# Optimization experiments

Hardware: AMD Instinct MI355X
Metric: run time of the kernel (lower is better)

## Reference

```python
import jax, jax.numpy as jnp
import numpy as np

D_MODEL = 1024
D_STATE = 16
D_CONV = 4
EXPAND = 2
D_INNER = D_MODEL * EXPAND


def soft_clamp(x, lo, hi, sharp):
    c = (hi + lo) / 2.0
    r = (hi - lo) / 2.0
    return jnp.tanh((x - c) / (r + 1e-8) * sharp) / sharp * r + c


def setup_inputs() -> dict:
    key = jax.random.key(0)
    ks = jax.random.split(key, 9)
    B, L = 2, 1024
    x = jax.random.normal(ks[0], (B, L, D_MODEL), jnp.float32)
    norm_w = jnp.ones((D_MODEL,), jnp.float32)
    W_in = jax.random.normal(ks[1], (2 * D_INNER, D_MODEL), jnp.float32) * 0.02
    conv_w = jax.random.normal(ks[2], (D_INNER, 1, D_CONV), jnp.float32) * 0.02
    conv_b = jnp.zeros((D_INNER,), jnp.float32)
    W_dt = jax.random.normal(ks[3], (D_INNER, D_INNER), jnp.float32) * 0.02
    b_dt = jnp.full((D_INNER,), -2.0, jnp.float32)
    W_B = jax.random.normal(ks[4], (D_STATE, D_INNER), jnp.float32) * 0.02
    W_C = jax.random.normal(ks[5], (D_STATE, D_INNER), jnp.float32) * 0.02
    A_log = jax.random.normal(ks[6], (D_INNER, D_STATE), jnp.float32) * 0.1
    D_param = jnp.full((D_INNER,), 0.1, jnp.float32)
    W_out = jax.random.normal(ks[7], (D_MODEL, D_INNER), jnp.float32) * 0.02
    residual_scale = jnp.asarray(0.3, jnp.float32)
    return dict(x=x, norm_w=norm_w, W_in=W_in, conv_w=conv_w, conv_b=conv_b,
                W_dt=W_dt, b_dt=b_dt, W_B=W_B, W_C=W_C, A_log=A_log,
                D_param=D_param, W_out=W_out, residual_scale=residual_scale)


def reference(x, norm_w, W_in, conv_w, conv_b, W_dt, b_dt, W_B, W_C, A_log,
              D_param, W_out, residual_scale):
    B, L, _ = x.shape
    # RMSNorm
    var = jnp.mean(x * x, axis=-1, keepdims=True)
    xn = x * jax.lax.rsqrt(var + 1e-6) * norm_w
    # in_proj, chunk into ssm branch and gate branch
    proj = xn @ W_in.T                              # (B, L, 2*D_INNER)
    x_branch, gate = proj[..., :D_INNER], proj[..., D_INNER:]
    # depthwise causal conv1d (padding=d_conv-1 then slice == left pad)
    xc = jax.lax.conv_general_dilated(
        jnp.swapaxes(x_branch, 1, 2), conv_w, (1,), [(D_CONV - 1, 0)],
        dimension_numbers=('NCH', 'OIH', 'NCH'), feature_group_count=D_INNER)
    xc = xc + conv_b[None, :, None]
    xc = jnp.swapaxes(xc, 1, 2)                     # (B, L, D_INNER)
    xc = xc * jax.nn.sigmoid(xc)                    # SiLU
    # selective SSM parameterization
    dt = soft_clamp(jax.nn.softplus(xc @ W_dt.T + b_dt), 1e-3, 0.1, 0.5)
    Bp = xc @ W_B.T                                 # (B, L, N)
    Cp = xc @ W_C.T                                 # (B, L, N)
    A = -jnp.exp(soft_clamp(A_log, -5.0, 5.0, 0.5))  # (D, N)
    dt_A = soft_clamp(dt[..., None] * A[None, None], -8.0, 8.0, 0.5)
    dA = jnp.exp(dt_A)                              # (B, L, D, N)
    dB = dt[..., None] * Bp[:, :, None, :]          # (B, L, D, N)

    h0 = jnp.zeros((B, D_INNER, D_STATE), jnp.float32)

    def step(h, inp):
        dA_t, dB_t, x_t, C_t, t = inp
        h = h * dA_t + dB_t * x_t[:, :, None]
        # every 10 steps: rescale if ||h|| > 20 (factor==1 otherwise)
        nrm = jnp.sqrt(jnp.sum(h * h, axis=(1, 2), keepdims=True))
        fac = jnp.minimum(20.0 / (nrm + 1e-8), 1.0)
        h = jnp.where(t % 10 == 0, h * fac, h)
        y = jnp.einsum('bdn,bn->bd', h, C_t) + D_param * x_t
        return h, y

    xs = (jnp.swapaxes(dA, 0, 1), jnp.swapaxes(dB, 0, 1),
          jnp.swapaxes(xc, 0, 1), jnp.swapaxes(Cp, 0, 1), jnp.arange(L))
    _, ys = jax.lax.scan(step, h0, xs)
    x_ssm = jnp.swapaxes(ys, 0, 1)                  # (B, L, D_INNER)

    x_out = (x_ssm * (gate * jax.nn.sigmoid(gate))) @ W_out.T
    scale = jax.nn.sigmoid(residual_scale) * 0.5
    return x + scale * x_out
```

## Files before the change

### kernel.cpp

```cpp
#include <hip/hip_runtime.h>
#include <hip/hip_bf16.h>
#include <math.h>

#define B_   2
#define L_   1024
#define DM   1024
#define DI   2048
#define DS   16
#define M_   (B_*L_)
#define TCH  64
#define NCH  16
#define NCHAIN (B_*DI*DS)

typedef __hip_bfloat16 bf16;
typedef __attribute__((ext_vector_type(8))) short short8;
typedef __attribute__((ext_vector_type(4))) float f32x4;

__device__ __forceinline__ float bf2f(bf16 v){ return __bfloat162float(v); }
__device__ __forceinline__ bf16  f2bf(float v){ return __float2bfloat16(v); }
__device__ __forceinline__ float s2f(short v){ bf16 b; *(short*)&b = v; return bf2f(b); }
__device__ __forceinline__ short f2s(float v){ bf16 b = f2bf(v); return *(short*)&b; }

__device__ __forceinline__ float ftanh(float x){
  float e = __expf(-2.f*fabsf(x));
  float t = (1.f-e)/(1.f+e);
  return x < 0.f ? -t : t;
}
__device__ __forceinline__ float fsoftplus(float x){
  return fmaxf(x,0.f) + log1pf(__expf(-fabsf(x)));
}
__device__ __forceinline__ float soft_clamp(float x, float lo, float hi){
  float c = 0.5f*(hi+lo), r = 0.5f*(hi-lo);
  float u = (x-c)/(r+1e-8f)*0.5f;
  return ftanh(u)*2.f*r + c;
}

#define NT 13
struct SrcPtrs { const void* p[NT]; };

static constexpr size_t CUM[NT+1] = {
  0,
  2097152,
  2098176,
  6292480,
  6300672,
  6302720,
  10497024,
  10499072,
  10531840,
  10564608,
  10597376,
  10599424,
  12696576,
  12696577
};
#define TOTELEM 12696577
#define CVTBLK  ((TOTELEM - 2097152 + 255)/256)

__global__ __launch_bounds__(256) void prep_k(SrcPtrs sp, bf16* __restrict__ arena,
                                              bf16* __restrict__ xn){
  __shared__ float wsum[4];
  const bool isbf = (((const unsigned short*)sp.p[1])[0] == 0x3F80u);
  if (blockIdx.x < M_){
    const int row = blockIdx.x;
    const int t   = threadIdx.x;
    float f[4];
    if (isbf){
      const bf16* xr = (const bf16*)sp.p[0] + (size_t)row*DM;
      #pragma unroll
      for (int i=0;i<4;i++) f[i] = bf2f(xr[t*4+i]);
    } else {
      const float* xr = (const float*)sp.p[0] + (size_t)row*DM;
      f32x4 v = *(const f32x4*)&xr[t*4];
      #pragma unroll
      for (int i=0;i<4;i++) f[i] = v[i];
    }
    float ss = f[0]*f[0]+f[1]*f[1]+f[2]*f[2]+f[3]*f[3];
    #pragma unroll
    for (int s=32;s;s>>=1) ss += __shfl_xor(ss, s, 64);
    if ((t & 63) == 0) wsum[t>>6] = ss;
    __syncthreads();
    float tot = wsum[0]+wsum[1]+wsum[2]+wsum[3];
    float rr  = rsqrtf(tot*(1.f/DM) + 1e-6f);
    float wv[4];
    if (isbf){
      const bf16* wp = (const bf16*)sp.p[1];
      #pragma unroll
      for (int i=0;i<4;i++) wv[i] = bf2f(wp[t*4+i]);
    } else {
      f32x4 v = *(const f32x4*)((const float*)sp.p[1] + t*4);
      #pragma unroll
      for (int i=0;i<4;i++) wv[i] = v[i];
    }
    bf16* o = xn + (size_t)row*DM;
    #pragma unroll
    for (int i=0;i<4;i++) o[t*4+i] = f2bf(f[i]*rr*wv[i]);
  } else {
    size_t i = (size_t)(blockIdx.x - M_)*256 + threadIdx.x + CUM[1];
    if (i >= TOTELEM) return;
    int s = 1;
    #pragma unroll
    for (int k=2;k<NT;k++) if (i >= CUM[k]) s = k;
    size_t loc = i - CUM[s];
    float v = isbf ? bf2f(((const bf16*)sp.p[s])[loc])
                   : ((const float*)sp.p[s])[loc];
    arena[i] = f2bf(v);
  }
}

__device__ __forceinline__ void gload16(const bf16* g, short* l){
  __builtin_amdgcn_global_load_lds((const __attribute__((address_space(1))) void*)g,
                                   (__attribute__((address_space(3))) void*)l, 16, 0, 0);
}

template<int EPI, int BM, int BN, int WR, int WC>
__global__ __launch_bounds__(256)
void gemm_bt(const bf16* __restrict__ A, const bf16* __restrict__ Bw,
             bf16* __restrict__ Cb,
             const int M, const int Ncols, const int K,
             const bf16* __restrict__ bias,
             const void* __restrict__ xraw,
             const bf16* __restrict__ rsp,
             void* __restrict__ outraw,
             const unsigned short* __restrict__ probe,
             float* __restrict__ BpOut, float* __restrict__ CpOut){
  constexpr int WM   = BM/WR, WN = BN/WC;
  constexpr int MI   = WM/16, NJ = WN/16;
  constexpr int ROWS = BM + BN;
  constexpr int STG  = ROWS*32/2048;
  __shared__ __align__(16) short ls[2][ROWS*32];
  const int tid  = threadIdx.x;
  const int lane = tid & 63;
  const int w    = tid >> 6;
  const int wr   = (w / WC) * WM;
  const int wc   = (w % WC) * WN;
  const int lc   = lane & 15;
  const int kb   = (lane >> 4) * 8;
  int bx, by;
  if (EPI == 1){
    const int flat = blockIdx.x;
    if (flat < 512){ bx = flat & 31; by = flat >> 5; }
    else           { bx = 32;        by = flat - 512; }
  } else { bx = blockIdx.x; by = blockIdx.y; }
  const int m0   = by * BM;
  const int n0   = bx * BN;

  auto stage = [&](int kk, int b){
    #pragma unroll
    for (int r=0;r<STG;r++){
      const int idx = r*2048 + tid*8;
      const int row = idx >> 5, col = idx & 31;
      const bf16* src = (row < BM) ? (A  + (size_t)(m0 + row)*K + kk + col)
                                   : (Bw + (size_t)(n0 + row - BM)*K + kk + col);
      gload16(src, &ls[b][idx]);
    }
  };

  f32x4 acc[MI][NJ] = {};

  stage(0, 0);
  int cur = 0;
  for (int k0 = 0; k0 < K; k0 += 32){
    __syncthreads();
    if (k0 + 32 < K) stage(k0 + 32, cur^1);
    short8 af[MI], bfv[NJ];
    #pragma unroll
    for (int i=0;i<MI;i++) af[i]  = *(const short8*)&ls[cur][(wr + i*16 + lc)*32 + kb];
    #pragma unroll
    for (int j=0;j<NJ;j++) bfv[j] = *(const short8*)&ls[cur][(BM + wc + j*16 + lc)*32 + kb];
    #pragma unroll
    for (int i=0;i<MI;i++)
      #pragma unroll
      for (int j=0;j<NJ;j++)
        acc[i][j] = __builtin_amdgcn_mfma_f32_16x16x32_bf16(af[i], bfv[j], acc[i][j], 0, 0, 0);
    cur ^= 1;
  }

  const int lr = lane >> 4;
  float scale = 0.f;
  bool isbf = true;
  if (EPI == 2){
    scale = 0.5f / (1.f + __expf(-bf2f(rsp[0])));
    isbf  = (probe[0] == 0x3F80u);
  }
  #pragma unroll
  for (int i=0;i<MI;i++){
    #pragma unroll
    for (int j=0;j<NJ;j++){
      const int gm0 = m0 + wr + i*16 + lr*4;
      const int gn  = n0 + wc + j*16 + lc;
      #pragma unroll
      for (int r=0;r<4;r++){
        float v = acc[i][j][r];
        const int gm = gm0 + r;
        if (EPI == 0){
          Cb[(size_t)gm*Ncols + gn] = f2bf(v);
        } else if (EPI == 1){
          if (gn < 2048){
            float z = fsoftplus(v + bf2f(bias[gn]));
            Cb[(size_t)gm*2048 + gn] = f2bf(soft_clamp(z, 0.001f, 0.1f));
          } else if (gn >= 2049 && gn < 2065){
            BpOut[gm*16 + (gn-2049)] = v;
          } else if (gn >= 2065 && gn < 2081){
            CpOut[gm*16 + (gn-2065)] = v;
          }
        } else {
          size_t off = (size_t)gm*Ncols + gn;
          if (isbf){
            float xv = bf2f(((const bf16*)xraw)[off]);
            ((bf16*)outraw)[off] = f2bf(xv + scale*v);
          } else {
            float xv = ((const float*)xraw)[off];
            ((float*)outraw)[off] = xv + scale*v;
          }
        }
      }
    }
  }
}

__global__ __launch_bounds__(256) void conv_silu_k(const bf16* __restrict__ proj,
                                                   const bf16* __restrict__ cw,
                                                   const bf16* __restrict__ cb,
                                                   bf16* __restrict__ xc){
  const int idx8 = blockIdx.x*256 + threadIdx.x;
  const int dp   = idx8 & (DI/8 - 1);
  const int row  = idx8 >> 8;
  const int l    = row & (L_-1);
  const int d0   = dp*8;
  short8 vb = *(const short8*)&cb[d0];
  short8 w0 = *(const short8*)&cw[d0*4];
  short8 w1 = *(const short8*)&cw[d0*4+8];
  short8 w2 = *(const short8*)&cw[d0*4+16];
  short8 w3 = *(const short8*)&cw[d0*4+24];
  float s[8];
  #pragma unroll
  for (int i=0;i<8;i++) s[i] = s2f(vb[i]);
  #pragma unroll
  for (int k=0;k<4;k++){
    int ll = l - 3 + k;
    if (ll >= 0){
      short8 vp = *(const short8*)&proj[(size_t)(row-3+k)*(2*DI) + d0];
      #pragma unroll
      for (int i=0;i<8;i++){
        const int widx = i*4+k;
        short wv = (widx<8)?w0[widx]:(widx<16)?w1[widx-8]:(widx<24)?w2[widx-16]:w3[widx-24];
        s[i] += s2f(vp[i])*s2f(wv);
      }
    }
  }
  short8 o;
  #pragma unroll
  for (int i=0;i<8;i++) o[i] = f2s(s[i] / (1.f + __expf(-s[i])));
  *(short8*)&xc[(size_t)idx8*8] = o;
}


__global__ __launch_bounds__(64) void scanA_k(const bf16* __restrict__ dtab,
    const bf16* __restrict__ xcb, const float* __restrict__ Bp,
    const bf16* __restrict__ Alog,
    float* __restrict__ Pg, float* __restrict__ Qg){
  __shared__ __align__(16) bf16  sdt[TCH][72];
  __shared__ __align__(16) bf16  sxc[TCH][72];
  __shared__ __align__(16) float sB [TCH][16];
  const int bx   = blockIdx.x;
  const int c    = bx & 15;
  const int dti  = (bx >> 4) & 31;
  const int b    = bx >> 9;
  const int lane = threadIdx.x;
  const int d0   = dti*64, d = d0 + lane;
  const int t0   = c*TCH;
  const size_t bL = (size_t)b*L_;
  #pragma unroll
  for (int i=0;i<8;i++){
    int task = i*64 + lane;
    int t = task >> 3, sub = task & 7;
    size_t g = (bL + t0 + t)*DI + d0 + sub*8;
    *(short8*)&sdt[t][sub*8] = *(const short8*)&dtab[g];
    *(short8*)&sxc[t][sub*8] = *(const short8*)&xcb[g];
  }
  #pragma unroll
  for (int i=0;i<4;i++){
    int task = i*64 + lane;
    int t = task >> 2, sub = task & 3;
    *(f32x4*)&sB[t][sub*4] = *(const f32x4*)&Bp[(bL + t0 + t)*DS + sub*4];
  }
  float Av[16];
  #pragma unroll
  for (int n=0;n<16;n++)
    Av[n] = -__expf(soft_clamp(bf2f(Alog[(size_t)d*DS + n]), -5.f, 5.f));
  __syncthreads();

  float P[16], Q[16];
  #pragma unroll
  for (int n=0;n<16;n++){ P[n]=1.f; Q[n]=0.f; }
  for (int t=0;t<TCH;t++){
    float dtv = bf2f(sdt[t][lane]);
    float xv  = bf2f(sxc[t][lane]);
    float dtx = dtv*xv;
    #pragma unroll
    for (int n=0;n<16;n++){
      float a = __expf(dtv*Av[n]);
      P[n] *= a;
      Q[n] = a*Q[n] + dtx*sB[t][n];
    }
  }
  const size_t base = ((size_t)c*(B_*DI) + (size_t)b*DI + d)*DS;
  #pragma unroll
  for (int n=0;n<16;n+=4){
    f32x4 pv = {P[n],P[n+1],P[n+2],P[n+3]};
    f32x4 qv = {Q[n],Q[n+1],Q[n+2],Q[n+3]};
    *(f32x4*)&Pg[base+n] = pv;
    *(f32x4*)&Qg[base+n] = qv;
  }
}

__global__ __launch_bounds__(64) void scanBC_k(const bf16* __restrict__ dtab,
    const bf16* __restrict__ xcb, const float* __restrict__ Bp,
    const float* __restrict__ Cp, const bf16* __restrict__ Alog,
    const bf16* __restrict__ Dp,
    const float* __restrict__ Pg, const float* __restrict__ Qg,
    const bf16* __restrict__ proj, bf16* __restrict__ aout){
  __shared__ __align__(16) bf16  sdt[TCH][72];
  __shared__ __align__(16) bf16  sxc[TCH][72];
  __shared__ __align__(16) bf16  sg [TCH][72];
  __shared__ __align__(16) float sB [TCH][16];
  __shared__ __align__(16) float sC [TCH][16];
  const int bx   = blockIdx.x;
  const int c    = bx & 15;
  const int dti  = (bx >> 4) & 31;
  const int b    = bx >> 9;
  const int lane = threadIdx.x;
  const int d0   = dti*64, d = d0 + lane;
  const int t0   = c*TCH;
  const size_t bL = (size_t)b*L_;
  #pragma unroll
  for (int i=0;i<8;i++){
    int task = i*64 + lane;
    int t = task >> 3, sub = task & 7;
    size_t g = (bL + t0 + t)*DI + d0 + sub*8;
    *(short8*)&sdt[t][sub*8] = *(const short8*)&dtab[g];
    *(short8*)&sxc[t][sub*8] = *(const short8*)&xcb[g];
    *(short8*)&sg [t][sub*8] = *(const short8*)&proj[(bL + t0 + t)*(2*DI) + DI + d0 + sub*8];
  }
  #pragma unroll
  for (int i=0;i<4;i++){
    int task = i*64 + lane;
    int t = task >> 2, sub = task & 3;
    *(f32x4*)&sB[t][sub*4] = *(const f32x4*)&Bp[(bL + t0 + t)*DS + sub*4];
    *(f32x4*)&sC[t][sub*4] = *(const f32x4*)&Cp[(bL + t0 + t)*DS + sub*4];
  }
  float Av[16];
  #pragma unroll
  for (int n=0;n<16;n++)
    Av[n] = -__expf(soft_clamp(bf2f(Alog[(size_t)d*DS + n]), -5.f, 5.f));
  float h[16];
  #pragma unroll
  for (int n=0;n<16;n++) h[n] = 0.f;
  const size_t chainb = ((size_t)b*DI + d)*DS;
  for (int cc=0; cc<c; cc++){
    const size_t pb = (size_t)cc*(B_*DI*DS) + chainb;
    #pragma unroll
    for (int n=0;n<16;n+=4){
      f32x4 pv = *(const f32x4*)&Pg[pb+n];
      f32x4 qv = *(const f32x4*)&Qg[pb+n];
      #pragma unroll
      for (int k=0;k<4;k++) h[n+k] = pv[k]*h[n+k] + qv[k];
    }
  }
  const float Dv = bf2f(Dp[d]);
  __syncthreads();

  for (int t=0;t<TCH;t++){
    float dtv = bf2f(sdt[t][lane]);
    float xv  = bf2f(sxc[t][lane]);
    float dtx = dtv*xv;
    float y   = Dv*xv;
    #pragma unroll
    for (int n=0;n<16;n++){
      float a = __expf(dtv*Av[n]);
      h[n] = a*h[n] + dtx*sB[t][n];
      y   += h[n]*sC[t][n];
    }
    float gv  = bf2f(sg[t][lane]);
    float sig = 1.f/(1.f + __expf(-gv));
    aout[(bL + t0 + t)*DI + d] = f2bf(y * gv * sig);
  }
}

extern "C" void kernel_launch(void* const* d_in, const int* in_sizes, int n_in,
                              void* d_out, int out_size, void* d_ws, size_t ws_size,
                              hipStream_t stream) {
  SrcPtrs sp;
  for (int i=0;i<NT;i++) sp.p[i] = d_in[i];

  char* ws = (char*)d_ws;
  bf16* arena = (bf16*)ws;  ws += ((size_t)TOTELEM*2 + 255) & ~(size_t)255;
  bf16*  proj = (bf16*)ws;  ws += (size_t)M_*2*DI*2;
  bf16*  xc   = (bf16*)ws;  ws += (size_t)M_*DI*2;
  bf16*  dt   = (bf16*)ws;  ws += (size_t)M_*DI*2;
  float* Bp   = (float*)ws; ws += (size_t)M_*DS*4;
  float* Cp   = (float*)ws; ws += (size_t)M_*DS*4;
  float* Pg   = (float*)ws; ws += (size_t)NCH*NCHAIN*4;
  float* Qg   = (float*)ws; ws += (size_t)NCH*NCHAIN*4;
  bf16*  xn   = (bf16*)Qg;
  bf16*  aout = dt;

  bf16* Win_b  = arena + CUM[2];
  bf16* cw_b   = arena + CUM[3];
  bf16* cb_b   = arena + CUM[4];
  bf16* Wdt_b  = arena + CUM[5];
  bf16* bdt_b  = arena + CUM[6];
  bf16* Alog_b = arena + CUM[9];
  bf16* Dp_b   = arena + CUM[10];
  bf16* Wout_b = arena + CUM[11];
  bf16* rs_b   = arena + CUM[12];

  prep_k<<<M_ + CVTBLK, 256, 0, stream>>>(sp, arena, xn);
  gemm_bt<0,128,128,2,2><<<dim3(4096/128, M_/128), 256, 0, stream>>>(xn, Win_b, proj,
      M_, 2*DI, DM, nullptr, nullptr, nullptr, nullptr, nullptr, nullptr, nullptr);
  conv_silu_k<<<(M_*DI/8)/256, 256, 0, stream>>>(proj, cw_b, cb_b, xc);
  gemm_bt<1,128,64,2,2><<<528, 256, 0, stream>>>(xc, Wdt_b, dt,
      M_, 2048, DI, bdt_b, nullptr, nullptr, nullptr, nullptr, Bp, Cp);
  scanA_k<<<B_*32*NCH, 64, 0, stream>>>(dt, xc, Bp, Alog_b, Pg, Qg);
  scanBC_k<<<B_*32*NCH, 64, 0, stream>>>(dt, xc, Bp, Cp, Alog_b, Dp_b, Pg, Qg, proj, aout);
  gemm_bt<2,64,64,2,2><<<dim3(DM/64, M_/64), 256, 0, stream>>>(aout, Wout_b, nullptr,
      M_, DM, DI, nullptr, d_in[0], rs_b, d_out, (const unsigned short*)d_in[1], nullptr, nullptr);
}
```

Before: 307.7 us.

## Fuse chunked scan passes into one cooperative kernel with grid sync

Merges the two chunked-scan kernels into a single cooperative kernel. Each block computes its chunk's P/Q summary, then a grid-wide barrier separates that from the prefix and output phase, so the dt/xc/B tiles loaded into shared memory are reused instead of read twice. It also drops the shared-memory row padding, which can bring back bank conflicts, and reorders the dt-GEMM block mapping so the 16 edge-column blocks are scheduled first. The cooperative launch needs all 1024 blocks resident at once, and the grid sync adds its own cost.

```diff
diff --git a/kernel.cpp b/kernel.cpp
--- a/kernel.cpp
+++ b/kernel.cpp
@@ -1,6 +1,9 @@
 #include <hip/hip_runtime.h>
 #include <hip/hip_bf16.h>
+#include <hip/hip_cooperative_groups.h>
 #include <math.h>
+
+namespace cg = cooperative_groups;
 
 #define B_   2
 #define L_   1024
@@ -139,8 +142,8 @@
   int bx, by;
   if (EPI == 1){
     const int flat = blockIdx.x;
-    if (flat < 512){ bx = flat & 31; by = flat >> 5; }
-    else           { bx = 32;        by = flat - 512; }
+    if (flat < 16){ bx = 32; by = flat; }
+    else          { const int f = flat - 16; bx = f & 31; by = f >> 5; }
   } else { bx = blockIdx.x; by = blockIdx.y; }
   const int m0   = by * BM;
   const int n0   = bx * BN;
@@ -255,75 +258,15 @@
   *(short8*)&xc[(size_t)idx8*8] = o;
 }
 
-
-__global__ __launch_bounds__(64) void scanA_k(const bf16* __restrict__ dtab,
-    const bf16* __restrict__ xcb, const float* __restrict__ Bp,
-    const bf16* __restrict__ Alog,
-    float* __restrict__ Pg, float* __restrict__ Qg){
-  __shared__ __align__(16) bf16  sdt[TCH][72];
-  __shared__ __align__(16) bf16  sxc[TCH][72];
-  __shared__ __align__(16) float sB [TCH][16];
-  const int bx   = blockIdx.x;
-  const int c    = bx & 15;
-  const int dti  = (bx >> 4) & 31;
-  const int b    = bx >> 9;
-  const int lane = threadIdx.x;
-  const int d0   = dti*64, d = d0 + lane;
-  const int t0   = c*TCH;
-  const size_t bL = (size_t)b*L_;
-  #pragma unroll
-  for (int i=0;i<8;i++){
-    int task = i*64 + lane;
-    int t = task >> 3, sub = task & 7;
-    size_t g = (bL + t0 + t)*DI + d0 + sub*8;
-    *(short8*)&sdt[t][sub*8] = *(const short8*)&dtab[g];
-    *(short8*)&sxc[t][sub*8] = *(const short8*)&xcb[g];
-  }
-  #pragma unroll
-  for (int i=0;i<4;i++){
-    int task = i*64 + lane;
-    int t = task >> 2, sub = task & 3;
-    *(f32x4*)&sB[t][sub*4] = *(const f32x4*)&Bp[(bL + t0 + t)*DS + sub*4];
-  }
-  float Av[16];
-  #pragma unroll
-  for (int n=0;n<16;n++)
-    Av[n] = -__expf(soft_clamp(bf2f(Alog[(size_t)d*DS + n]), -5.f, 5.f));
-  __syncthreads();
-
-  float P[16], Q[16];
-  #pragma unroll
-  for (int n=0;n<16;n++){ P[n]=1.f; Q[n]=0.f; }
-  for (int t=0;t<TCH;t++){
-    float dtv = bf2f(sdt[t][lane]);
-    float xv  = bf2f(sxc[t][lane]);
-    float dtx = dtv*xv;
-    #pragma unroll
-    for (int n=0;n<16;n++){
-      float a = __expf(dtv*Av[n]);
-      P[n] *= a;
-      Q[n] = a*Q[n] + dtx*sB[t][n];
-    }
-  }
-  const size_t base = ((size_t)c*(B_*DI) + (size_t)b*DI + d)*DS;
-  #pragma unroll
-  for (int n=0;n<16;n+=4){
-    f32x4 pv = {P[n],P[n+1],P[n+2],P[n+3]};
-    f32x4 qv = {Q[n],Q[n+1],Q[n+2],Q[n+3]};
-    *(f32x4*)&Pg[base+n] = pv;
-    *(f32x4*)&Qg[base+n] = qv;
-  }
-}
-
-__global__ __launch_bounds__(64) void scanBC_k(const bf16* __restrict__ dtab,
+__global__ __launch_bounds__(64) void scanF_k(const bf16* __restrict__ dtab,
     const bf16* __restrict__ xcb, const float* __restrict__ Bp,
     const float* __restrict__ Cp, const bf16* __restrict__ Alog,
     const bf16* __restrict__ Dp,
-    const float* __restrict__ Pg, const float* __restrict__ Qg,
+    float* __restrict__ Pg, float* __restrict__ Qg,
     const bf16* __restrict__ proj, bf16* __restrict__ aout){
-  __shared__ __align__(16) bf16  sdt[TCH][72];
-  __shared__ __align__(16) bf16  sxc[TCH][72];
-  __shared__ __align__(16) bf16  sg [TCH][72];
+  __shared__ __align__(16) bf16  sdt[TCH][64];
+  __shared__ __align__(16) bf16  sxc[TCH][64];
+  __shared__ __align__(16) bf16  sg [TCH][64];
   __shared__ __align__(16) float sB [TCH][16];
   __shared__ __align__(16) float sC [TCH][16];
   const int bx   = blockIdx.x;
@@ -354,12 +297,40 @@
   #pragma unroll
   for (int n=0;n<16;n++)
     Av[n] = -__expf(soft_clamp(bf2f(Alog[(size_t)d*DS + n]), -5.f, 5.f));
+  const float Dv = bf2f(Dp[d]);
+  __syncthreads();
+
+  float P[16], Q[16];
+  #pragma unroll
+  for (int n=0;n<16;n++){ P[n]=1.f; Q[n]=0.f; }
+  for (int t=0;t<TCH;t++){
+    float dtv = bf2f(sdt[t][lane]);
+    float xv  = bf2f(sxc[t][lane]);
+    float dtx = dtv*xv;
+    #pragma unroll
+    for (int n=0;n<16;n++){
+      float a = __expf(dtv*Av[n]);
+      P[n] *= a;
+      Q[n] = a*Q[n] + dtx*sB[t][n];
+    }
+  }
+  const size_t chainb = ((size_t)b*DI + d)*DS;
+  const size_t base = (size_t)c*NCHAIN + chainb;
+  #pragma unroll
+  for (int n=0;n<16;n+=4){
+    f32x4 pv = {P[n],P[n+1],P[n+2],P[n+3]};
+    f32x4 qv = {Q[n],Q[n+1],Q[n+2],Q[n+3]};
+    *(f32x4*)&Pg[base+n] = pv;
+    *(f32x4*)&Qg[base+n] = qv;
+  }
+
+  cg::this_grid().sync();
+
   float h[16];
   #pragma unroll
   for (int n=0;n<16;n++) h[n] = 0.f;
-  const size_t chainb = ((size_t)b*DI + d)*DS;
   for (int cc=0; cc<c; cc++){
-    const size_t pb = (size_t)cc*(B_*DI*DS) + chainb;
+    const size_t pb = (size_t)cc*NCHAIN + chainb;
     #pragma unroll
     for (int n=0;n<16;n+=4){
       f32x4 pv = *(const f32x4*)&Pg[pb+n];
@@ -368,9 +339,6 @@
       for (int k=0;k<4;k++) h[n+k] = pv[k]*h[n+k] + qv[k];
     }
   }
-  const float Dv = bf2f(Dp[d]);
-  __syncthreads();
-
   for (int t=0;t<TCH;t++){
     float dtv = bf2f(sdt[t][lane]);
     float xv  = bf2f(sxc[t][lane]);
@@ -422,8 +390,15 @@
   conv_silu_k<<<(M_*DI/8)/256, 256, 0, stream>>>(proj, cw_b, cb_b, xc);
   gemm_bt<1,128,64,2,2><<<528, 256, 0, stream>>>(xc, Wdt_b, dt,
       M_, 2048, DI, bdt_b, nullptr, nullptr, nullptr, nullptr, Bp, Cp);
-  scanA_k<<<B_*32*NCH, 64, 0, stream>>>(dt, xc, Bp, Alog_b, Pg, Qg);
-  scanBC_k<<<B_*32*NCH, 64, 0, stream>>>(dt, xc, Bp, Cp, Alog_b, Dp_b, Pg, Qg, proj, aout);
+  {
+    const bf16* a0 = dt;   const bf16* a1 = xc;  const float* a2 = Bp;
+    const float* a3 = Cp;  const bf16* a4 = Alog_b; const bf16* a5 = Dp_b;
+    float* a6 = Pg;        float* a7 = Qg;       const bf16* a8 = proj;
+    bf16* a9 = aout;
+    void* kargs[] = {&a0,&a1,&a2,&a3,&a4,&a5,&a6,&a7,&a8,&a9};
+    hipLaunchCooperativeKernel((const void*)scanF_k, dim3(B_*32*NCH), dim3(64),
+                               kargs, 0, stream);
+  }
   gemm_bt<2,64,64,2,2><<<dim3(DM/64, M_/64), 256, 0, stream>>>(aout, Wout_b, nullptr,
       M_, DM, DI, nullptr, d_in[0], rs_b, d_out, (const unsigned short*)d_in[1], nullptr, nullptr);
 }
```

Measured after the change: 422.0 us. 1.37x slower.
